# Performance work log

Measured on AMD Instinct MI355X. Metric: run time of the kernel, lower is better.

Reference implementation:

```python
import jax, jax.numpy as jnp
import numpy as np

VOCAB = 30522
BZ, SEQ, D, P = 32, 2048, 768, 16
PLACEHOLDER_ID = 1
UNK_ID = 100


def setup_inputs() -> dict:
    key = jax.random.key(0)
    k1, k2, k3, k4 = jax.random.split(key, 4)
    # random token ids, guaranteed != PLACEHOLDER_ID
    input_ids = jax.random.randint(k1, (BZ, SEQ), UNK_ID + 1, VOCAB)
    # choose exactly P distinct placeholder positions per row (module requires this)
    pos = jnp.argsort(jax.random.uniform(k2, (BZ, SEQ)), axis=1)[:, :P]
    input_ids = input_ids.at[jnp.arange(BZ)[:, None], pos].set(PLACEHOLDER_ID)
    emb_table = jax.random.normal(k3, (VOCAB, D), jnp.float32) * 0.02
    prompt = jax.random.normal(k4, (P, D), jnp.float32)
    return {"input_ids": input_ids, "emb_table": emb_table, "prompt": prompt}


def reference(input_ids, emb_table, prompt):
    # mask of placeholder positions; exactly P per row
    mask = input_ids == PLACEHOLDER_ID                         # [BZ, SEQ]
    # placeholder tokens are looked up as UNK, then overwritten by prompt rows
    emb = emb_table[jnp.where(mask, UNK_ID, input_ids)]        # [BZ, SEQ, D]
    # i-th placeholder (in sequence order) gets prompt[i] -> rank via cumsum
    rank = jnp.clip(jnp.cumsum(mask, axis=1) - 1, 0, P - 1)    # [BZ, SEQ]
    out = jnp.where(mask[:, :, None], prompt[rank], emb)       # [BZ, SEQ, D]
    return out
```

## Files before the change

### kernel.cpp

```cpp
#include <hip/hip_runtime.h>
#include <hip/hip_bf16.h>

#define VOCAB 30522
#define BZ 32
#define SEQ 2048
#define D 768
#define P 16
#define PLACEHOLDER_ID 1

typedef float f32x4 __attribute__((ext_vector_type(4)));

__global__ void rank_kernel(const int* __restrict__ ids, int* __restrict__ rank) {
    const int b = blockIdx.x;
    const int t = threadIdx.x;
    constexpr int CHUNK = SEQ / 256;
    const int* row = ids + (size_t)b * SEQ;
    const int base = t * CHUNK;

    int m[CHUNK];
    int cnt = 0;
#pragma unroll
    for (int i = 0; i < CHUNK; ++i) {
        m[i] = (row[base + i] == PLACEHOLDER_ID) ? 1 : 0;
        cnt += m[i];
    }

    const int lane = t & 63;
    const int wave = t >> 6;
    int incl = cnt;
#pragma unroll
    for (int off = 1; off < 64; off <<= 1) {
        int v = __shfl_up(incl, off, 64);
        if (lane >= off) incl += v;
    }
    __shared__ int wsum[4];
    if (lane == 63) wsum[wave] = incl;
    __syncthreads();
    int woff = 0;
    for (int w = 0; w < wave; ++w) woff += wsum[w];

    int run = woff + (incl - cnt);
    int* rrow = rank + (size_t)b * SEQ;
#pragma unroll
    for (int i = 0; i < CHUNK; ++i) {
        run += m[i];
        int r = run - 1;
        r = r < 0 ? 0 : (r > (P - 1) ? (P - 1) : r);
        rrow[base + i] = r;
    }
}

#define ROWS_PER_BLOCK 16
__global__ __launch_bounds__(256) void gather_kernel(
        const int* __restrict__ ids,
        const float* __restrict__ emb,
        const float* __restrict__ prompt,
        const int* __restrict__ rank,
        float* __restrict__ out) {
    constexpr int NF4 = D / 4;
    constexpr int F4_PER_BLOCK = ROWS_PER_BLOCK * NF4;
    constexpr int ITERS = F4_PER_BLOCK / 256;

    const int t = threadIdx.x;
    const int row0 = blockIdx.x * ROWS_PER_BLOCK;

    __shared__ const f32x4* srcs[ROWS_PER_BLOCK];
    if (t < ROWS_PER_BLOCK) {
        const int id = ids[row0 + t];
        srcs[t] = (id == PLACEHOLDER_ID)
                      ? (const f32x4*)(prompt + (size_t)rank[row0 + t] * D)
                      : (const f32x4*)(emb + (size_t)id * D);
    }
    __syncthreads();

    f32x4* dst = (f32x4*)(out + (size_t)row0 * D);

    f32x4 v[ITERS];
#pragma unroll
    for (int k = 0; k < ITERS; ++k) {
        const int f = k * 256 + t;
        const int r = f / NF4;
        const int c = f - r * NF4;
        v[k] = srcs[r][c];
    }
#pragma unroll
    for (int k = 0; k < ITERS; ++k) {
        __builtin_nontemporal_store(v[k], &dst[k * 256 + t]);
    }
}

extern "C" void kernel_launch(void* const* d_in, const int* in_sizes, int n_in,
                              void* d_out, int out_size, void* d_ws, size_t ws_size,
                              hipStream_t stream) {
    const int*   ids    = (const int*)d_in[0];
    const float* emb    = (const float*)d_in[1];
    const float* prompt = (const float*)d_in[2];
    float*       out    = (float*)d_out;
    int*         rank   = (int*)d_ws;

    rank_kernel<<<BZ, 256, 0, stream>>>(ids, rank);
    gather_kernel<<<(BZ * SEQ) / ROWS_PER_BLOCK, 256, 0, stream>>>(
        ids, emb, prompt, rank, out);
}
```

Measured before the change: 67.01 us.

## Fuse placeholder rank computation into gather kernel with on-demand prefix count

Removes the separate rank kernel and its workspace round trip. Each gather block checks whether any of its rows is a placeholder. Only those blocks recount placeholders in the preceding part of the row with a block reduction, then add the in-block prefix. This saves a kernel launch and the serial dependency between the two kernels, at the cost of redundant prefix scans in the few blocks that contain placeholders.

```diff
diff --git a/kernel.cpp b/kernel.cpp
--- a/kernel.cpp
+++ b/kernel.cpp
@@ -7,74 +7,69 @@
 #define D 768
 #define P 16
 #define PLACEHOLDER_ID 1
+#define ROWS_PER_BLOCK 16
 
 typedef float f32x4 __attribute__((ext_vector_type(4)));
 
-__global__ void rank_kernel(const int* __restrict__ ids, int* __restrict__ rank) {
-    const int b = blockIdx.x;
-    const int t = threadIdx.x;
-    constexpr int CHUNK = SEQ / 256;
-    const int* row = ids + (size_t)b * SEQ;
-    const int base = t * CHUNK;
-
-    int m[CHUNK];
-    int cnt = 0;
-#pragma unroll
-    for (int i = 0; i < CHUNK; ++i) {
-        m[i] = (row[base + i] == PLACEHOLDER_ID) ? 1 : 0;
-        cnt += m[i];
-    }
-
-    const int lane = t & 63;
-    const int wave = t >> 6;
-    int incl = cnt;
-#pragma unroll
-    for (int off = 1; off < 64; off <<= 1) {
-        int v = __shfl_up(incl, off, 64);
-        if (lane >= off) incl += v;
-    }
-    __shared__ int wsum[4];
-    if (lane == 63) wsum[wave] = incl;
-    __syncthreads();
-    int woff = 0;
-    for (int w = 0; w < wave; ++w) woff += wsum[w];
-
-    int run = woff + (incl - cnt);
-    int* rrow = rank + (size_t)b * SEQ;
-#pragma unroll
-    for (int i = 0; i < CHUNK; ++i) {
-        run += m[i];
-        int r = run - 1;
-        r = r < 0 ? 0 : (r > (P - 1) ? (P - 1) : r);
-        rrow[base + i] = r;
-    }
-}
-
-#define ROWS_PER_BLOCK 16
-__global__ __launch_bounds__(256) void gather_kernel(
+__global__ __launch_bounds__(256) void fused_gather_kernel(
         const int* __restrict__ ids,
         const float* __restrict__ emb,
         const float* __restrict__ prompt,
-        const int* __restrict__ rank,
         float* __restrict__ out) {
     constexpr int NF4 = D / 4;
-    constexpr int F4_PER_BLOCK = ROWS_PER_BLOCK * NF4;
-    constexpr int ITERS = F4_PER_BLOCK / 256;
+    constexpr int ITERS = ROWS_PER_BLOCK * NF4 / 256;
 
     const int t = threadIdx.x;
     const int row0 = blockIdx.x * ROWS_PER_BLOCK;
+    const int b = row0 / SEQ;
+    const int s0 = row0 - b * SEQ;
 
+    __shared__ int blk_ids[ROWS_PER_BLOCK];
+    __shared__ int has_ph;
     __shared__ const f32x4* srcs[ROWS_PER_BLOCK];
+    __shared__ int wred[4];
+
+    if (t == 0) has_ph = 0;
+    __syncthreads();
     if (t < ROWS_PER_BLOCK) {
         const int id = ids[row0 + t];
-        srcs[t] = (id == PLACEHOLDER_ID)
-                      ? (const f32x4*)(prompt + (size_t)rank[row0 + t] * D)
-                      : (const f32x4*)(emb + (size_t)id * D);
+        blk_ids[t] = id;
+        if (id == PLACEHOLDER_ID) atomicOr(&has_ph, 1);
+    }
+    __syncthreads();
+
+    if (has_ph) {
+        const int* row = ids + (size_t)b * SEQ;
+        const int p0 = t * 8;
+        int cnt = 0;
+#pragma unroll
+        for (int i = 0; i < 8; ++i) {
+            const int p = p0 + i;
+            if (p < s0) cnt += (row[p] == PLACEHOLDER_ID) ? 1 : 0;
+        }
+#pragma unroll
+        for (int off = 32; off; off >>= 1) cnt += __shfl_xor(cnt, off, 64);
+        const int lane = t & 63, wave = t >> 6;
+        if (lane == 0) wred[wave] = cnt;
+        __syncthreads();
+        if (t < ROWS_PER_BLOCK) {
+            int run = wred[0] + wred[1] + wred[2] + wred[3];
+            for (int j = 0; j < t; ++j)
+                run += (blk_ids[j] == PLACEHOLDER_ID) ? 1 : 0;
+            int r = run > (P - 1) ? (P - 1) : run;
+            const int id = blk_ids[t];
+            srcs[t] = (id == PLACEHOLDER_ID)
+                          ? (const f32x4*)(prompt + (size_t)r * D)
+                          : (const f32x4*)(emb + (size_t)id * D);
+        }
+    } else {
+        if (t < ROWS_PER_BLOCK) {
+            srcs[t] = (const f32x4*)(emb + (size_t)blk_ids[t] * D);
+        }
     }
     __syncthreads();
 
     f32x4* dst = (f32x4*)(out + (size_t)row0 * D);
-
     f32x4 v[ITERS];
 #pragma unroll
     for (int k = 0; k < ITERS; ++k) {
@@ -96,9 +91,7 @@
     const float* emb    = (const float*)d_in[1];
     const float* prompt = (const float*)d_in[2];
     float*       out    = (float*)d_out;
-    int*         rank   = (int*)d_ws;
 
-    rank_kernel<<<BZ, 256, 0, stream>>>(ids, rank);
-    gather_kernel<<<(BZ * SEQ) / ROWS_PER_BLOCK, 256, 0, stream>>>(
-        ids, emb, prompt, rank, out);
+    fused_gather_kernel<<<(BZ * SEQ) / ROWS_PER_BLOCK, 256, 0, stream>>>(
+        ids, emb, prompt, out);
 }
```

After: 63.55 us. 1.05x faster.

## Bucket-sort output rows by source embedding row to improve gather locality

Applied to the files above, without the earlier changes.

Computes a source key per token (vocab id or prompt slot), builds a histogram over key buckets of 16 with atomics, scans it, and scatters row indices into a sorted order. The gather kernel then processes rows in source-sorted order, with a block-index swizzle across 8 groups, so that nearby workgroups read nearby embedding rows and cache reuse improves. The cost is three extra launches, a memset, and atomic contention on the histogram. Output writes also become scattered at row granularity instead of contiguous.

```diff
diff --git a/kernel.cpp b/kernel.cpp
--- a/kernel.cpp
+++ b/kernel.cpp
@@ -6,86 +6,134 @@
 #define SEQ 2048
 #define D 768
 #define P 16
-#define PLACEHOLDER_ID 1
+#define PH_ID 1
+#define NROWS (BZ * SEQ)
+#define NKEYS (VOCAB + P)
+#define NB ((NKEYS >> 4) + 1)
+#define RPB 16
 
 typedef float f32x4 __attribute__((ext_vector_type(4)));
 
-__global__ void rank_kernel(const int* __restrict__ ids, int* __restrict__ rank) {
+__global__ void srcid_kernel(const int* __restrict__ ids,
+                             int* __restrict__ srcid,
+                             int* __restrict__ hist) {
     const int b = blockIdx.x;
     const int t = threadIdx.x;
-    constexpr int CHUNK = SEQ / 256;
     const int* row = ids + (size_t)b * SEQ;
-    const int base = t * CHUNK;
+    const int base = t * 8;
 
-    int m[CHUNK];
-    int cnt = 0;
+    int v[8], m[8], cnt = 0;
 #pragma unroll
-    for (int i = 0; i < CHUNK; ++i) {
-        m[i] = (row[base + i] == PLACEHOLDER_ID) ? 1 : 0;
+    for (int i = 0; i < 8; ++i) {
+        v[i] = row[base + i];
+        m[i] = (v[i] == PH_ID) ? 1 : 0;
         cnt += m[i];
     }
-
-    const int lane = t & 63;
-    const int wave = t >> 6;
+    const int lane = t & 63, wave = t >> 6;
     int incl = cnt;
 #pragma unroll
     for (int off = 1; off < 64; off <<= 1) {
-        int v = __shfl_up(incl, off, 64);
-        if (lane >= off) incl += v;
+        int x = __shfl_up(incl, off, 64);
+        if (lane >= off) incl += x;
     }
     __shared__ int wsum[4];
     if (lane == 63) wsum[wave] = incl;
     __syncthreads();
-    int woff = 0;
-    for (int w = 0; w < wave; ++w) woff += wsum[w];
+    int run = incl - cnt;
+    for (int w = 0; w < wave; ++w) run += wsum[w];
 
-    int run = woff + (incl - cnt);
-    int* rrow = rank + (size_t)b * SEQ;
+    int* srow = srcid + (size_t)b * SEQ;
 #pragma unroll
-    for (int i = 0; i < CHUNK; ++i) {
-        run += m[i];
-        int r = run - 1;
-        r = r < 0 ? 0 : (r > (P - 1) ? (P - 1) : r);
-        rrow[base + i] = r;
+    for (int i = 0; i < 8; ++i) {
+        int key;
+        if (m[i]) {
+            int r = run < (P - 1) ? run : (P - 1);
+            key = VOCAB + r;
+            ++run;
+        } else {
+            key = v[i];
+        }
+        srow[base + i] = key;
+        atomicAdd(&hist[key >> 4], 1);
     }
 }
 
-#define ROWS_PER_BLOCK 16
+__global__ void scan_kernel(int* __restrict__ hist) {
+    const int t = threadIdx.x;
+    int v[8], sum = 0;
+#pragma unroll
+    for (int i = 0; i < 8; ++i) {
+        const int idx = t * 8 + i;
+        v[i] = (idx < NB) ? hist[idx] : 0;
+        sum += v[i];
+    }
+    const int lane = t & 63, wave = t >> 6;
+    int incl = sum;
+#pragma unroll
+    for (int off = 1; off < 64; off <<= 1) {
+        int x = __shfl_up(incl, off, 64);
+        if (lane >= off) incl += x;
+    }
+    __shared__ int wsum[4];
+    if (lane == 63) wsum[wave] = incl;
+    __syncthreads();
+    int run = incl - sum;
+    for (int w = 0; w < wave; ++w) run += wsum[w];
+#pragma unroll
+    for (int i = 0; i < 8; ++i) {
+        const int idx = t * 8 + i;
+        if (idx < NB) { hist[idx] = run; run += v[i]; }
+    }
+}
+
+__global__ void scatter_kernel(const int* __restrict__ srcid,
+                               int* __restrict__ hist,
+                               int* __restrict__ sorted) {
+    const int i = blockIdx.x * 256 + threadIdx.x;
+    const int key = srcid[i];
+    const int pos = atomicAdd(&hist[key >> 4], 1);
+    sorted[pos] = i;
+}
+
 __global__ __launch_bounds__(256) void gather_kernel(
-        const int* __restrict__ ids,
+        const int* __restrict__ srcid,
+        const int* __restrict__ sorted,
         const float* __restrict__ emb,
         const float* __restrict__ prompt,
-        const int* __restrict__ rank,
         float* __restrict__ out) {
     constexpr int NF4 = D / 4;
-    constexpr int F4_PER_BLOCK = ROWS_PER_BLOCK * NF4;
-    constexpr int ITERS = F4_PER_BLOCK / 256;
+    constexpr int ITERS = RPB * NF4 / 256;
+    constexpr int NWG = NROWS / RPB;
 
+    const int bid = blockIdx.x;
+    const int chunk = (bid & 7) * (NWG / 8) + (bid >> 3);
+    const int g0 = chunk * RPB;
     const int t = threadIdx.x;
-    const int row0 = blockIdx.x * ROWS_PER_BLOCK;
 
-    __shared__ const f32x4* srcs[ROWS_PER_BLOCK];
-    if (t < ROWS_PER_BLOCK) {
-        const int id = ids[row0 + t];
-        srcs[t] = (id == PLACEHOLDER_ID)
-                      ? (const f32x4*)(prompt + (size_t)rank[row0 + t] * D)
-                      : (const f32x4*)(emb + (size_t)id * D);
+    __shared__ const f32x4* s_src[RPB];
+    __shared__ f32x4* s_dst[RPB];
+    if (t < RPB) {
+        const int r = sorted[g0 + t];
+        const int k = srcid[r];
+        s_src[t] = (k >= VOCAB)
+                       ? (const f32x4*)(prompt + (size_t)(k - VOCAB) * D)
+                       : (const f32x4*)(emb + (size_t)k * D);
+        s_dst[t] = (f32x4*)(out + (size_t)r * D);
     }
     __syncthreads();
 
-    f32x4* dst = (f32x4*)(out + (size_t)row0 * D);
-
     f32x4 v[ITERS];
+    int rr[ITERS], cc[ITERS];
 #pragma unroll
     for (int k = 0; k < ITERS; ++k) {
         const int f = k * 256 + t;
-        const int r = f / NF4;
-        const int c = f - r * NF4;
-        v[k] = srcs[r][c];
+        rr[k] = f / NF4;
+        cc[k] = f - rr[k] * NF4;
+        v[k] = s_src[rr[k]][cc[k]];
     }
 #pragma unroll
     for (int k = 0; k < ITERS; ++k) {
-        __builtin_nontemporal_store(v[k], &dst[k * 256 + t]);
+        __builtin_nontemporal_store(v[k], &s_dst[rr[k]][cc[k]]);
     }
 }
 
@@ -96,9 +144,14 @@
     const float* emb    = (const float*)d_in[1];
     const float* prompt = (const float*)d_in[2];
     float*       out    = (float*)d_out;
-    int*         rank   = (int*)d_ws;
 
-    rank_kernel<<<BZ, 256, 0, stream>>>(ids, rank);
-    gather_kernel<<<(BZ * SEQ) / ROWS_PER_BLOCK, 256, 0, stream>>>(
-        ids, emb, prompt, rank, out);
+    int* hist   = (int*)d_ws;
+    int* srcid  = hist + NB;
+    int* sorted = srcid + NROWS;
+
+    hipMemsetAsync(hist, 0, NB * sizeof(int), stream);
+    srcid_kernel<<<BZ, 256, 0, stream>>>(ids, srcid, hist);
+    scan_kernel<<<1, 256, 0, stream>>>(hist);
+    scatter_kernel<<<NROWS / 256, 256, 0, stream>>>(srcid, hist, sorted);
+    gather_kernel<<<NROWS / RPB, 256, 0, stream>>>(srcid, sorted, emb, prompt, out);
 }
```

New measurement: 79.66 us. 18.9% more time.
